# Kernel optimization log

Measured on AMD Instinct MI355X. Metric: run time of the kernel, lower is better.

## Reference

```python
import jax, jax.numpy as jnp
import numpy as np

# Dimensions
N, C, D, H = 4, 1024, 768, 12      # docs, seq_len, hidden, heads
E, M, P = 32, 4, 256               # entities/doc, mentions/entity, pairs/doc
BS, NL = 64, 97                    # block_size, num relation labels


def setup_inputs() -> dict:
    key = jax.random.key(0)
    ks = jax.random.split(key, 16)
    s = 0.02
    seq = jax.random.normal(ks[0], (N, C, D), jnp.float32)
    attn = jax.random.uniform(ks[1], (N, H, C, C), jnp.float32)
    pos = jax.random.randint(ks[2], (N, E, M), 1, C)         # mention positions (offset applied, all valid)
    hts = jax.random.randint(ks[3], (N, P, 2), 0, E)         # entity-pair indices
    return {
        'seq': seq, 'attn': attn, 'pos': pos, 'hts': hts,
        'Wq': jax.random.normal(ks[4], (D, D), jnp.float32) * s,
        'bq': jnp.zeros((D,), jnp.float32),
        'Wk': jax.random.normal(ks[5], (D, D), jnp.float32) * s,
        'bk': jnp.zeros((D,), jnp.float32),
        'aw': jax.random.normal(ks[6], (2 * D, 1), jnp.float32) * s,
        'ab': jnp.zeros((1,), jnp.float32),
        'Wh': jax.random.normal(ks[7], (3 * D, D), jnp.float32) * s,
        'bh': jnp.zeros((D,), jnp.float32),
        'Wt': jax.random.normal(ks[8], (3 * D, D), jnp.float32) * s,
        'bt': jnp.zeros((D,), jnp.float32),
        'Wb': jax.random.normal(ks[9], (D * BS, NL), jnp.float32) * s,
        'bb': jnp.zeros((NL,), jnp.float32),
    }


def mention_guide(rs, mem, mask, Wq, bq, Wk, bk, aw, ab):
    # rs: [N,P,D] query; mem: [N,P,M,D] mention embs; mask: [N,P,M] bool
    sq = rs @ Wq + bq                                  # [N,P,D]
    sk = mem @ Wk + bk                                 # [N,P,M,D]
    sq_exp = jnp.broadcast_to(sq[:, :, None, :], sk.shape)
    inp = jnp.concatenate([sq_exp, sk], axis=-1)       # [N,P,M,2D]
    scores = jax.nn.leaky_relu((inp @ aw + ab)[..., 0], 0.01)   # [N,P,M]
    scores = jnp.where(mask, scores, -1e9)
    p = jax.nn.softmax(scores, axis=-1)                # attention over mentions
    return jnp.einsum('npm,npmd->npd', p, sk)


def reference(seq, attn, pos, hts, Wq, bq, Wk, bk, aw, ab, Wh, bh, Wt, bt, Wb, bb):
    nidx = jnp.arange(N)
    # per-entity mention gather + logsumexp pooling
    ment_emb = seq[nidx[:, None, None], pos]                      # [N,E,M,D]
    ent_emb = jax.scipy.special.logsumexp(ment_emb, axis=2)       # [N,E,D]
    att_t = attn.transpose(0, 2, 1, 3)                            # [N,C,H,C]
    ent_att = att_t[nidx[:, None, None], pos].mean(axis=2)        # [N,E,H,C]

    h_idx, t_idx = hts[..., 0], hts[..., 1]
    b = nidx[:, None]
    hs = ent_emb[b, h_idx]                                        # [N,P,D]
    ts = ent_emb[b, t_idx]
    h_att = ent_att[b, h_idx]                                     # [N,P,H,C]
    t_att = ent_att[b, t_idx]
    ht_att = (h_att * t_att).mean(axis=2)                         # [N,P,C]
    ht_att = ht_att / (ht_att.sum(axis=-1, keepdims=True) + 1e-5)
    rs = jnp.einsum('ncd,npc->npd', seq, ht_att)                  # local context

    # mention-level attention for head/tail entities
    h_pos = pos[b, h_idx]                                         # [N,P,M]
    t_pos = pos[b, t_idx]
    h_embs = seq[nidx[:, None, None], h_pos]                      # [N,P,M,D]
    t_embs = seq[nidx[:, None, None], t_pos]
    hess = mention_guide(rs, h_embs, h_pos != 0, Wq, bq, Wk, bk, aw, ab)
    tess = mention_guide(rs, t_embs, t_pos != 0, Wq, bq, Wk, bk, aw, ab)

    zh = jnp.tanh(jnp.tanh(jnp.concatenate([rs, hs, hess], -1) @ Wh + bh))
    zt = jnp.tanh(jnp.concatenate([rs, ts, tess], -1) @ Wt + bt)

    # group bilinear classifier
    b1 = zh.reshape(N * P, D // BS, BS)
    b2 = zt.reshape(N * P, D // BS, BS)
    bl = (b1[:, :, :, None] * b2[:, :, None, :]).reshape(N * P, D * BS)
    return bl @ Wb + bb                                            # [N*P, NL]
```

## Files before the change

kernel.cpp:

```cpp
#include <hip/hip_runtime.h>
#include <hip/hip_bf16.h>
#include <math.h>

#define N_ 4
#define C_ 1024
#define D_ 768
#define H_ 12
#define E_ 32
#define M_ 4
#define P_ 256
#define NL_ 97
#define NLP_ 112
#define NP_ (N_*P_)
#define K3D_ 2304
#define KBL_ 49152

typedef __attribute__((ext_vector_type(8))) short short8;
typedef __attribute__((ext_vector_type(4))) float f32x4;
typedef __attribute__((ext_vector_type(4))) unsigned short ushort4v;

__device__ __forceinline__ short f2bf(float x){
  union { __hip_bfloat16 h; short s; } u; u.h = __float2bfloat16(x); return u.s;
}
__device__ __forceinline__ unsigned short f2bfu(float x){
  union { __hip_bfloat16 h; unsigned short s; } u; u.h = __float2bfloat16(x); return u.s;
}
__device__ __forceinline__ float bf2f(unsigned short u){
  union { unsigned int i; float f; } x; x.i = ((unsigned int)u)<<16; return x.f;
}

__device__ __forceinline__ float blockReduceSum256(float v){
  __shared__ float red_s[4];
  #pragma unroll
  for (int o=32;o>0;o>>=1) v += __shfl_down(v, o);
  if ((threadIdx.x & 63)==0) red_s[threadIdx.x>>6] = v;
  __syncthreads();
  float t = red_s[0]+red_s[1]+red_s[2]+red_s[3];
  __syncthreads();
  return t;
}

__device__ __forceinline__ void tcvt64(const float* __restrict__ in,
    __hip_bfloat16* __restrict__ out, int R, int C, int Cp, int tile){
  __shared__ float tb[64][33];
  const int tiles_c = (Cp + 31) >> 5;
  const int rb = (tile/tiles_c)*64, cb = (tile%tiles_c)*32;
  const int tid = threadIdx.x;
  const bool vec = ((C & 3) == 0);
  #pragma unroll
  for (int i=0;i<2;i++){
    const int idx = tid + i*256;
    const int row = idx>>3, c4 = (idx&7)*4;
    const int c = cb + c4;
    float v0=0.f,v1=0.f,v2=0.f,v3=0.f;
    if (vec && c+3 < C){
      const f32x4 v = *(const f32x4*)&in[(size_t)(rb+row)*C + c];
      v0=v[0]; v1=v[1]; v2=v[2]; v3=v[3];
    } else {
      const float* rp = in + (size_t)(rb+row)*C;
      if (c   < C) v0 = rp[c];
      if (c+1 < C) v1 = rp[c+1];
      if (c+2 < C) v2 = rp[c+2];
      if (c+3 < C) v3 = rp[c+3];
    }
    tb[row][c4]=v0; tb[row][c4+1]=v1; tb[row][c4+2]=v2; tb[row][c4+3]=v3;
  }
  __syncthreads();
  #pragma unroll
  for (int i=0;i<4;i++){
    const int idx = tid + i*256;
    const int cr = idx>>5, p = idx&31;
    const int cc = cb + cr;
    if (cc < Cp){
      union { struct { unsigned short a,b; } s; unsigned int u; } pk;
      pk.s.a = f2bfu(tb[2*p][cr]);
      pk.s.b = f2bfu(tb[2*p+1][cr]);
      *(unsigned int*)&out[(size_t)cc*R + rb + 2*p] = pk.u;
    }
  }
}

#define T_WH 864
#define T_WT 864
#define T_WK 288
#define T_WB 3072
#define T_SEQ 1536
#define O_WT  (T_WH)
#define O_WK  (O_WT+T_WT)
#define O_WB  (O_WK+T_WK)
#define O_SEQ (O_WB+T_WB)
#define O_EMB (O_SEQ+T_SEQ)
#define O_ATT (O_EMB+N_*E_)
#define O_VQ  (O_ATT+N_*E_*H_)
#define O_WKAW (O_VQ+D_)
#define O_MISC (O_WKAW+D_)
#define G_PREP (O_MISC+1)

__global__ __launch_bounds__(256) void k_prep(
    const float* __restrict__ seq, const float* __restrict__ attn,
    const int* __restrict__ pos,
    const float* __restrict__ Wq, const float* __restrict__ bq,
    const float* __restrict__ Wk, const float* __restrict__ bk,
    const float* __restrict__ aw, const float* __restrict__ ab,
    const float* __restrict__ Wh, const float* __restrict__ Wt,
    const float* __restrict__ Wb,
    __hip_bfloat16* __restrict__ WhT, __hip_bfloat16* __restrict__ WtT,
    __hip_bfloat16* __restrict__ WkT, __hip_bfloat16* __restrict__ WbT,
    __hip_bfloat16* __restrict__ seqT,
    __hip_bfloat16* __restrict__ ent_bf, __hip_bfloat16* __restrict__ Ambf,
    __hip_bfloat16* __restrict__ att_bf,
    float* __restrict__ vq, float* __restrict__ wk_aw, float* __restrict__ qc2){
  const int b = blockIdx.x;
  const int tid = threadIdx.x;
  if (b < O_WT){ tcvt64(Wh, WhT, K3D_, D_, D_, b); return; }
  if (b < O_WK){ tcvt64(Wt, WtT, K3D_, D_, D_, b-O_WT); return; }
  if (b < O_WB){ tcvt64(Wk, WkT, D_, D_, D_, b-O_WK); return; }
  if (b < O_SEQ){ tcvt64(Wb, WbT, KBL_, NL_, NLP_, b-O_WB); return; }
  if (b < O_EMB){ tcvt64(seq, seqT, N_*C_, D_, D_, b-O_SEQ); return; }
  if (b < O_ATT){
    const int be = b - O_EMB;
    const int n = be >> 5;
    const int* pp = pos + be*M_;
    if (tid < 192){
      const int c4 = tid*4;
      const f32x4 v0 = *(const f32x4*)&seq[((size_t)n*C_ + pp[0])*D_ + c4];
      const f32x4 v1 = *(const f32x4*)&seq[((size_t)n*C_ + pp[1])*D_ + c4];
      const f32x4 v2 = *(const f32x4*)&seq[((size_t)n*C_ + pp[2])*D_ + c4];
      const f32x4 v3 = *(const f32x4*)&seq[((size_t)n*C_ + pp[3])*D_ + c4];
      ushort4v a0,a1,a2,a3,e;
      #pragma unroll
      for (int j=0;j<4;j++){
        a0[j]=f2bfu(v0[j]); a1[j]=f2bfu(v1[j]); a2[j]=f2bfu(v2[j]); a3[j]=f2bfu(v3[j]);
        const float m = fmaxf(fmaxf(v0[j],v1[j]), fmaxf(v2[j],v3[j]));
        const float s = expf(v0[j]-m)+expf(v1[j]-m)+expf(v2[j]-m)+expf(v3[j]-m);
        e[j] = f2bfu(m + logf(s));
      }
      *(ushort4v*)&Ambf[(size_t)(be*4+0)*D_ + c4] = a0;
      *(ushort4v*)&Ambf[(size_t)(be*4+1)*D_ + c4] = a1;
      *(ushort4v*)&Ambf[(size_t)(be*4+2)*D_ + c4] = a2;
      *(ushort4v*)&Ambf[(size_t)(be*4+3)*D_ + c4] = a3;
      *(ushort4v*)&ent_bf[(size_t)be*D_ + c4] = e;
    }
    return;
  }
  if (b < O_VQ){
    const int bb2 = b - O_ATT;
    const int h = bb2 % H_;
    const int ne = bb2 / H_;
    const int n = ne >> 5;
    const int* pp = pos + ne*M_;
    const float* basep = attn + ((size_t)(n*H_+h))*C_*C_;
    const int c4 = tid*4;
    const f32x4 r0 = *(const f32x4*)&basep[(size_t)pp[0]*C_ + c4];
    const f32x4 r1 = *(const f32x4*)&basep[(size_t)pp[1]*C_ + c4];
    const f32x4 r2 = *(const f32x4*)&basep[(size_t)pp[2]*C_ + c4];
    const f32x4 r3 = *(const f32x4*)&basep[(size_t)pp[3]*C_ + c4];
    ushort4v o;
    #pragma unroll
    for (int j=0;j<4;j++) o[j] = f2bfu(0.25f*(r0[j]+r1[j]+r2[j]+r3[j]));
    *(ushort4v*)&att_bf[(size_t)bb2*C_ + c4] = o;
    return;
  }
  if (b < O_WKAW){
    const int k = b - O_VQ;
    float s = 0.f;
    for (int d=tid; d<D_; d+=256) s += Wq[(size_t)k*D_+d]*aw[d];
    s = blockReduceSum256(s);
    if (tid==0) vq[k] = s;
    return;
  }
  if (b < O_MISC){
    const int k = b - O_WKAW;
    float s = 0.f;
    for (int d=tid; d<D_; d+=256) s += Wk[(size_t)k*D_+d]*aw[D_+d];
    s = blockReduceSum256(s);
    if (tid==0) wk_aw[k] = s;
    return;
  }
  {
    float s0 = 0.f, s1 = 0.f;
    for (int d=tid; d<D_; d+=256){ s0 += bq[d]*aw[d]; s1 += bk[d]*aw[D_+d]; }
    s0 = blockReduceSum256(s0);
    s1 = blockReduceSum256(s1);
    if (tid==0){ qc2[0] = s0 + ab[0]; qc2[1] = s1; }
  }
}

__global__ __launch_bounds__(256) void k_ht2(
    const __hip_bfloat16* __restrict__ att_bf, const int* __restrict__ hts,
    const __hip_bfloat16* __restrict__ Ambf, const float* __restrict__ wk_aw,
    const float* __restrict__ qc2,
    __hip_bfloat16* __restrict__ ht_bf, float* __restrict__ kdot){
  const int b = blockIdx.x, tid = threadIdx.x;
  if (b < NP_){
    const int r = b, n = r >> 8;
    const int he = hts[r*2], te = hts[r*2+1];
    const unsigned short* ha = (const unsigned short*)att_bf + ((size_t)(n*E_+he))*H_*C_;
    const unsigned short* ta = (const unsigned short*)att_bf + ((size_t)(n*E_+te))*H_*C_;
    const int c0 = tid*4;
    float v[4] = {0.f,0.f,0.f,0.f};
    #pragma unroll
    for (int h=0;h<H_;h++){
      const ushort4v a = *(const ushort4v*)&ha[h*C_ + c0];
      const ushort4v t = *(const ushort4v*)&ta[h*C_ + c0];
      #pragma unroll
      for (int j=0;j<4;j++) v[j] = fmaf(bf2f(a[j]), bf2f(t[j]), v[j]);
    }
    float local = 0.f;
    #pragma unroll
    for (int j=0;j<4;j++){ v[j] *= (1.0f/H_); local += v[j]; }
    const float tot = blockReduceSum256(local);
    const float inv = 1.f/(tot + 1e-5f);
    ushort4v o;
    #pragma unroll
    for (int j=0;j<4;j++) o[j] = f2bfu(v[j]*inv);
    *(ushort4v*)&ht_bf[(size_t)r*C_ + c0] = o;
  } else {
    const int g = b - NP_;
    const unsigned short* Am = (const unsigned short*)Ambf + (size_t)g*D_;
    float s = 0.f;
    for (int d=tid; d<D_; d+=256) s += bf2f(Am[d])*wk_aw[d];
    s = blockReduceSum256(s);
    if (tid==0) kdot[g] = s + qc2[1];
  }
}

__global__ __launch_bounds__(256) void k_gemm1(
    const __hip_bfloat16* __restrict__ Ambf, const __hip_bfloat16* __restrict__ WkT,
    const float* __restrict__ bk, float* __restrict__ KK,
    const __hip_bfloat16* __restrict__ ht_bf, const __hip_bfloat16* __restrict__ seqT,
    __hip_bfloat16* __restrict__ rs_bf){
  __shared__ short As[64][136];
  __shared__ short Bs[64][136];
  const int tid = threadIdx.x;
  const int w = tid>>6, l = tid&63, wm = w>>1, wn = w&1;
  const int srow = tid>>4, sk8 = (tid&15)*8;
  const short *Ap, *Bp;
  int lda, ldb, K, bm, bn;
  bool isKK;
  if (blockIdx.x < 96){
    isKK = true;
    bm = (blockIdx.x/12)*64; bn = (blockIdx.x%12)*64;
    Ap = (const short*)Ambf + (size_t)bm*D_; lda = D_; K = D_;
    Bp = (const short*)WkT + (size_t)bn*D_;  ldb = D_;
  } else {
    isKK = false;
    const int z = blockIdx.x - 96;
    const int n = z/48, rem = z%48, bmI = rem/12, bnI = rem%12;
    bm = n*P_ + bmI*64; bn = bnI*64;
    Ap = (const short*)ht_bf + (size_t)bm*C_;            lda = C_;     K = C_;
    Bp = (const short*)seqT + (size_t)bn*(N_*C_) + n*C_; ldb = N_*C_;
  }
  short8 pA[4], pB[4];
  auto loadAB = [&](int k0){
    #pragma unroll
    for (int t=0;t<4;t++){
      const int row = srow + t*16;
      pA[t] = *(const short8*)&Ap[(size_t)row*lda + k0 + sk8];
      pB[t] = *(const short8*)&Bp[(size_t)row*ldb + k0 + sk8];
    }
  };
  loadAB(0);
  f32x4 acc[2][2] = {};
  for (int k0=0;k0<K;k0+=128){
    #pragma unroll
    for (int t=0;t<4;t++){
      *(short8*)&As[srow+t*16][sk8] = pA[t];
      *(short8*)&Bs[srow+t*16][sk8] = pB[t];
    }
    __syncthreads();
    if (k0+128 < K) loadAB(k0+128);
    #pragma unroll
    for (int h=0;h<4;h++){
      short8 af[2], bfv[2];
      #pragma unroll
      for (int f=0;f<2;f++){
        af[f]  = *(short8*)&As[wm*32+f*16+(l&15)][h*32+(l>>4)*8];
        bfv[f] = *(short8*)&Bs[wn*32+f*16+(l&15)][h*32+(l>>4)*8];
      }
      #pragma unroll
      for (int i=0;i<2;i++)
        #pragma unroll
        for (int j=0;j<2;j++)
          acc[i][j] = __builtin_amdgcn_mfma_f32_16x16x32_bf16(af[i], bfv[j], acc[i][j], 0,0,0);
    }
    __syncthreads();
  }
  #pragma unroll
  for (int i=0;i<2;i++)
    #pragma unroll
    for (int j=0;j<2;j++)
      #pragma unroll
      for (int r_=0;r_<4;r_++){
        const int row = bm + wm*32 + i*16 + (l>>4)*4 + r_;
        const int col = bn + wn*32 + j*16 + (l&15);
        const float v = acc[i][j][r_];
        if (isKK) KK[(size_t)row*D_ + col] = v + bk[col];
        else      rs_bf[(size_t)row*D_ + col] = __float2bfloat16(v);
      }
}

__global__ __launch_bounds__(256) void k_mention(
    const __hip_bfloat16* __restrict__ rs_bf, const float* __restrict__ KK,
    const float* __restrict__ vq, const float* __restrict__ qc2,
    const float* __restrict__ kdot, const int* __restrict__ pos,
    const int* __restrict__ hts,
    __hip_bfloat16* __restrict__ hess, __hip_bfloat16* __restrict__ tess){
  const int r = blockIdx.x, n = r>>8, tid = threadIdx.x;
  const unsigned short* rsp = (const unsigned short*)rs_bf + (size_t)r*D_;
  float s = 0.f;
  for (int d=tid; d<D_; d+=256) s += bf2f(rsp[d])*vq[d];
  const float q = blockReduceSum256(s) + qc2[0];
  #pragma unroll
  for (int side=0;side<2;side++){
    const int e = hts[r*2+side];
    const int base = (n*E_+e)*M_;
    float sc[4];
    #pragma unroll
    for (int m=0;m<4;m++){
      float t = q + kdot[base+m];
      t = (t > 0.f) ? t : 0.01f*t;
      sc[m] = (pos[base+m] != 0) ? t : -1e9f;
    }
    const float mx = fmaxf(fmaxf(sc[0],sc[1]), fmaxf(sc[2],sc[3]));
    float ex[4]; float sum = 0.f;
    #pragma unroll
    for (int m=0;m<4;m++){ ex[m] = expf(sc[m]-mx); sum += ex[m]; }
    const float inv = 1.f/sum;
    const float p0=ex[0]*inv, p1=ex[1]*inv, p2=ex[2]*inv, p3=ex[3]*inv;
    const float* K0 = KK + (size_t)(base+0)*D_;
    const float* K1 = KK + (size_t)(base+1)*D_;
    const float* K2 = KK + (size_t)(base+2)*D_;
    const float* K3 = KK + (size_t)(base+3)*D_;
    __hip_bfloat16* outp = (side ? tess : hess) + (size_t)r*D_;
    for (int d=tid; d<D_; d+=256)
      outp[d] = __float2bfloat16(p0*K0[d] + p1*K1[d] + p2*K2[d] + p3*K3[d]);
  }
}

__global__ __launch_bounds__(256) void k_gemm_z(
    const __hip_bfloat16* __restrict__ rs_bf, const __hip_bfloat16* __restrict__ ent_bf,
    const __hip_bfloat16* __restrict__ hess_bf, const __hip_bfloat16* __restrict__ tess_bf,
    const int* __restrict__ hts,
    const __hip_bfloat16* __restrict__ WhT, const __hip_bfloat16* __restrict__ WtT,
    const float* __restrict__ bh, const float* __restrict__ bt,
    float* __restrict__ zh, float* __restrict__ zt){
  const int side = blockIdx.z;
  const int bm = blockIdx.y*64, bn = blockIdx.x*64;
  const short* BT = (const short*)(side ? WtT : WhT);
  const float* bias = side ? bt : bh;
  float* Cm = side ? zt : zh;
  const short* hx  = (const short*)(side ? tess_bf : hess_bf);
  const short* rsp = (const short*)rs_bf;
  const short* enp = (const short*)ent_bf;
  __shared__ short As[64][136];
  __shared__ short Bs[64][136];
  __shared__ int e_s[64];
  const int tid = threadIdx.x;
  if (tid < 64) e_s[tid] = hts[(bm+tid)*2 + side];
  __syncthreads();
  const int w = tid>>6, l = tid&63, wm = w>>1, wn = w&1;
  const int srow = tid>>4, sk8 = (tid&15)*8;
  short8 pA[4], pB[4];
  auto loadAB = [&](int k0){
    #pragma unroll
    for (int t=0;t<4;t++){
      const int row = srow + t*16;
      const int arow = bm + row;
      const int gk = k0 + sk8;
      const short* src;
      if (gk < D_)        src = &rsp[(size_t)arow*D_ + gk];
      else if (gk < 2*D_) src = &enp[((size_t)(arow>>8)*E_ + e_s[row])*D_ + gk - D_];
      else                src = &hx[(size_t)arow*D_ + gk - 2*D_];
      pA[t] = *(const short8*)src;
      pB[t] = *(const short8*)&BT[(size_t)(bn+row)*K3D_ + gk];
    }
  };
  loadAB(0);
  f32x4 acc[2][2] = {};
  for (int k0=0;k0<K3D_;k0+=128){
    #pragma unroll
    for (int t=0;t<4;t++){
      *(short8*)&As[srow+t*16][sk8] = pA[t];
      *(short8*)&Bs[srow+t*16][sk8] = pB[t];
    }
    __syncthreads();
    if (k0+128 < K3D_) loadAB(k0+128);
    #pragma unroll
    for (int h=0;h<4;h++){
      short8 af[2], bfv[2];
      #pragma unroll
      for (int f=0;f<2;f++){
        af[f]  = *(short8*)&As[wm*32+f*16+(l&15)][h*32+(l>>4)*8];
        bfv[f] = *(short8*)&Bs[wn*32+f*16+(l&15)][h*32+(l>>4)*8];
      }
      #pragma unroll
      for (int i=0;i<2;i++)
        #pragma unroll
        for (int j=0;j<2;j++)
          acc[i][j] = __builtin_amdgcn_mfma_f32_16x16x32_bf16(af[i], bfv[j], acc[i][j], 0,0,0);
    }
    __syncthreads();
  }
  #pragma unroll
  for (int i=0;i<2;i++)
    #pragma unroll
    for (int j=0;j<2;j++)
      #pragma unroll
      for (int r_=0;r_<4;r_++){
        const int row = bm + wm*32 + i*16 + (l>>4)*4 + r_;
        const int col = bn + wn*32 + j*16 + (l&15);
        float v = acc[i][j][r_] + bias[col];
        v = tanhf(v);
        if (side==0) v = tanhf(v);
        Cm[(size_t)row*D_ + col] = v;
      }
}

__global__ __launch_bounds__(256) void k_bilinear(
    const float* __restrict__ zh, const float* __restrict__ zt,
    const __hip_bfloat16* __restrict__ WbT, __hip_bfloat16* __restrict__ partial){
  const int kc = blockIdx.x;
  const int blkI = kc >> 1, half = kc & 1;
  const int r0 = blockIdx.y*64;
  __shared__ float zh_s[64][36];
  __shared__ float zt_s[64][68];
  __shared__ short Bs[4][NLP_][40];
  const int tid = threadIdx.x;
  for (int idx=tid; idx<64*32; idx+=256){
    const int row = idx>>5, c = idx&31;
    zh_s[row][c] = zh[(size_t)(r0+row)*D_ + blkI*64 + half*32 + c];
  }
  for (int idx=tid; idx<64*64; idx+=256){
    const int row = idx>>6, c = idx&63;
    zt_s[row][c] = zt[(size_t)(r0+row)*D_ + blkI*64 + c];
  }
  const int w = tid>>6, l = tid&63;
  const int arow = w*16 + (l&15);
  const short* WT = (const short*)WbT;
  const size_t kbase = (size_t)blkI*4096 + half*2048;
  int sl[7], cl[7], k8l[7];
  #pragma unroll
  for (int t=0;t<7;t++){
    const int ci = tid + t*256;
    sl[t] = ci/448;
    const int rem = ci - sl[t]*448;
    cl[t] = rem>>2; k8l[t] = (rem&3)*8;
  }
  short8 pre[7];
  #pragma unroll
  for (int t=0;t<7;t++)
    pre[t] = *(const short8*)&WT[(size_t)cl[t]*KBL_ + kbase + (size_t)sl[t]*32 + k8l[t]];
  f32x4 acc[7] = {};
  for (int g=0; g<16; ++g){
    __syncthreads();
    #pragma unroll
    for (int t=0;t<7;t++) *(short8*)&Bs[sl[t]][cl[t]][k8l[t]] = pre[t];
    __syncthreads();
    if (g < 15){
      #pragma unroll
      for (int t=0;t<7;t++)
        pre[t] = *(const short8*)&WT[(size_t)cl[t]*KBL_ + kbase + (size_t)((g+1)*4+sl[t])*32 + k8l[t]];
    }
    #pragma unroll
    for (int ss=0;ss<4;ss++){
      const int s = g*4 + ss;
      const int iLoc = s>>1;
      const int jj = (s&1)*32 + (l>>4)*8;
      const float a = zh_s[arow][iLoc];
      f32x4 z0 = *(f32x4*)&zt_s[arow][jj];
      f32x4 z1 = *(f32x4*)&zt_s[arow][jj+4];
      short8 afr;
      #pragma unroll
      for (int t=0;t<4;t++) afr[t]   = f2bf(a*z0[t]);
      #pragma unroll
      for (int t=0;t<4;t++) afr[4+t] = f2bf(a*z1[t]);
      #pragma unroll
      for (int nf=0;nf<7;nf++){
        const short8 bfr = *(short8*)&Bs[ss][nf*16 + (l&15)][(l>>4)*8];
        acc[nf] = __builtin_amdgcn_mfma_f32_16x16x32_bf16(afr, bfr, acc[nf], 0,0,0);
      }
    }
  }
  unsigned short* pp = (unsigned short*)partial;
  #pragma unroll
  for (int nf=0;nf<7;nf++)
    #pragma unroll
    for (int r_=0;r_<4;r_++){
      const int row = r0 + w*16 + (l>>4)*4 + r_;
      const int col = nf*16 + (l&15);
      pp[((size_t)kc*NP_ + row)*NLP_ + col] = f2bfu(acc[nf][r_]);
    }
}

__global__ __launch_bounds__(256) void k_reduce(const __hip_bfloat16* __restrict__ partial,
    const float* __restrict__ bb, float* __restrict__ out){
  const int idx = blockIdx.x*256 + threadIdx.x;
  if (idx >= NP_*NL_) return;
  const int r = idx / NL_;
  const int l = idx - r*NL_;
  const unsigned short* pp = (const unsigned short*)partial;
  float s = bb[l];
  #pragma unroll
  for (int kc=0;kc<24;kc++) s += bf2f(pp[((size_t)kc*NP_ + r)*NLP_ + l]);
  out[idx] = s;
}

extern "C" void kernel_launch(void* const* d_in, const int* in_sizes, int n_in,
                              void* d_out, int out_size, void* d_ws, size_t ws_size,
                              hipStream_t stream){
  const float* seq  = (const float*)d_in[0];
  const float* attn = (const float*)d_in[1];
  const int*   pos  = (const int*)d_in[2];
  const int*   hts  = (const int*)d_in[3];
  const float* Wq = (const float*)d_in[4];
  const float* bq = (const float*)d_in[5];
  const float* Wk = (const float*)d_in[6];
  const float* bk = (const float*)d_in[7];
  const float* aw = (const float*)d_in[8];
  const float* ab = (const float*)d_in[9];
  const float* Wh = (const float*)d_in[10];
  const float* bh = (const float*)d_in[11];
  const float* Wt = (const float*)d_in[12];
  const float* bt = (const float*)d_in[13];
  const float* Wb = (const float*)d_in[14];
  const float* bb = (const float*)d_in[15];
  float* out = (float*)d_out;

  char* base = (char*)d_ws;
  size_t off = 0;
  auto alloc = [&](size_t bytes)->void*{
    void* p = base + off;
    off += (bytes + 255) & ~(size_t)255;
    return p;
  };
  __hip_bfloat16* WhT   = (__hip_bfloat16*)alloc((size_t)D_*K3D_*2);
  __hip_bfloat16* WtT   = (__hip_bfloat16*)alloc((size_t)D_*K3D_*2);
  __hip_bfloat16* WkT   = (__hip_bfloat16*)alloc((size_t)D_*D_*2);
  __hip_bfloat16* WbT   = (__hip_bfloat16*)alloc((size_t)NLP_*KBL_*2);
  __hip_bfloat16* seqT  = (__hip_bfloat16*)alloc((size_t)D_*N_*C_*2);
  __hip_bfloat16* ent_bf= (__hip_bfloat16*)alloc((size_t)N_*E_*D_*2);
  __hip_bfloat16* att_bf= (__hip_bfloat16*)alloc((size_t)N_*E_*H_*C_*2);
  __hip_bfloat16* ht_bf = (__hip_bfloat16*)alloc((size_t)NP_*C_*2);
  __hip_bfloat16* Ambf  = (__hip_bfloat16*)alloc((size_t)N_*E_*M_*D_*2);
  float* KK             = (float*)alloc((size_t)N_*E_*M_*D_*4);
  float* vq             = (float*)alloc(D_*4);
  float* wk_aw          = (float*)alloc(D_*4);
  float* qc2            = (float*)alloc(256);
  float* kdot           = (float*)alloc(512*4);
  __hip_bfloat16* rs_bf = (__hip_bfloat16*)alloc((size_t)NP_*D_*2);
  __hip_bfloat16* hess  = (__hip_bfloat16*)alloc((size_t)NP_*D_*2);
  __hip_bfloat16* tess  = (__hip_bfloat16*)alloc((size_t)NP_*D_*2);
  float* zh             = (float*)alloc((size_t)NP_*D_*4);
  float* zt             = (float*)alloc((size_t)NP_*D_*4);
  __hip_bfloat16* partial = (__hip_bfloat16*)alloc((size_t)24*NP_*NLP_*2);
  (void)ws_size; (void)in_sizes; (void)n_in; (void)out_size;

  k_prep<<<G_PREP, 256, 0, stream>>>(seq, attn, pos, Wq, bq, Wk, bk, aw, ab, Wh, Wt, Wb,
                                     WhT, WtT, WkT, WbT, seqT, ent_bf, Ambf, att_bf,
                                     vq, wk_aw, qc2);
  k_ht2<<<NP_ + 512, 256, 0, stream>>>(att_bf, hts, Ambf, wk_aw, qc2, ht_bf, kdot);
  k_gemm1<<<288, 256, 0, stream>>>(Ambf, WkT, bk, KK, ht_bf, seqT, rs_bf);
  k_mention<<<NP_, 256, 0, stream>>>(rs_bf, KK, vq, qc2, kdot, pos, hts, hess, tess);
  k_gemm_z<<<dim3(D_/64, NP_/64, 2), 256, 0, stream>>>(rs_bf, ent_bf, hess, tess, hts,
                                                       WhT, WtT, bh, bt, zh, zt);
  k_bilinear<<<dim3(24, NP_/64), 256, 0, stream>>>(zh, zt, WbT, partial);
  k_reduce<<<(NP_*NL_+255)/256, 256, 0, stream>>>(partial, bb, out);
}
```

Measured before the change: 105.5 us.

## Split-K the z GEMM three ways and fuse reductions into bilinear via atomics

The z projection GEMM is split along K into three partial products (rs, entity, mention segments), giving 6x more blocks. The bias, tanh and summing of the partials move into the bilinear kernel's load phase. The separate reduce kernel is removed: the bilinear kernel atomically adds fp32 results into the output, which k_mention pre-initialises with the bias. This trades an extra kernel launch and a bf16 partial buffer for more fp32 partial traffic and atomic contention, and the atomic sums make results nondeterministic.

After: 117.3 us. +11.2%, slower.

```diff
diff --git a/kernel.cpp b/kernel.cpp
--- a/kernel.cpp
+++ b/kernel.cpp
@@ -305,8 +305,10 @@
     const float* __restrict__ vq, const float* __restrict__ qc2,
     const float* __restrict__ kdot, const int* __restrict__ pos,
     const int* __restrict__ hts,
-    __hip_bfloat16* __restrict__ hess, __hip_bfloat16* __restrict__ tess){
+    __hip_bfloat16* __restrict__ hess, __hip_bfloat16* __restrict__ tess,
+    const float* __restrict__ bb, float* __restrict__ out){
   const int r = blockIdx.x, n = r>>8, tid = threadIdx.x;
+  if (tid < NL_) out[(size_t)r*NL_ + tid] = bb[tid];
   const unsigned short* rsp = (const unsigned short*)rs_bf + (size_t)r*D_;
   float s = 0.f;
   for (int d=tid; d<D_; d+=256) s += bf2f(rsp[d])*vq[d];
@@ -343,16 +345,15 @@
     const __hip_bfloat16* __restrict__ hess_bf, const __hip_bfloat16* __restrict__ tess_bf,
     const int* __restrict__ hts,
     const __hip_bfloat16* __restrict__ WhT, const __hip_bfloat16* __restrict__ WtT,
-    const float* __restrict__ bh, const float* __restrict__ bt,
-    float* __restrict__ zh, float* __restrict__ zt){
-  const int side = blockIdx.z;
+    float* __restrict__ zp){
+  const int side = blockIdx.z & 1;
+  const int ks = blockIdx.z >> 1;
   const int bm = blockIdx.y*64, bn = blockIdx.x*64;
   const short* BT = (const short*)(side ? WtT : WhT);
-  const float* bias = side ? bt : bh;
-  float* Cm = side ? zt : zh;
   const short* hx  = (const short*)(side ? tess_bf : hess_bf);
   const short* rsp = (const short*)rs_bf;
   const short* enp = (const short*)ent_bf;
+  float* Cm = zp + (size_t)(side*3 + ks)*NP_*D_;
   __shared__ short As[64][136];
   __shared__ short Bs[64][136];
   __shared__ int e_s[64];
@@ -369,23 +370,23 @@
       const int arow = bm + row;
       const int gk = k0 + sk8;
       const short* src;
-      if (gk < D_)        src = &rsp[(size_t)arow*D_ + gk];
-      else if (gk < 2*D_) src = &enp[((size_t)(arow>>8)*E_ + e_s[row])*D_ + gk - D_];
-      else                src = &hx[(size_t)arow*D_ + gk - 2*D_];
+      if (ks == 0)      src = &rsp[(size_t)arow*D_ + gk];
+      else if (ks == 1) src = &enp[((size_t)(arow>>8)*E_ + e_s[row])*D_ + gk];
+      else              src = &hx[(size_t)arow*D_ + gk];
       pA[t] = *(const short8*)src;
-      pB[t] = *(const short8*)&BT[(size_t)(bn+row)*K3D_ + gk];
+      pB[t] = *(const short8*)&BT[(size_t)(bn+row)*K3D_ + ks*D_ + gk];
     }
   };
   loadAB(0);
   f32x4 acc[2][2] = {};
-  for (int k0=0;k0<K3D_;k0+=128){
+  for (int k0=0;k0<D_;k0+=128){
     #pragma unroll
     for (int t=0;t<4;t++){
       *(short8*)&As[srow+t*16][sk8] = pA[t];
       *(short8*)&Bs[srow+t*16][sk8] = pB[t];
     }
     __syncthreads();
-    if (k0+128 < K3D_) loadAB(k0+128);
+    if (k0+128 < D_) loadAB(k0+128);
     #pragma unroll
     for (int h=0;h<4;h++){
       short8 af[2], bfv[2];
@@ -410,16 +411,14 @@
       for (int r_=0;r_<4;r_++){
         const int row = bm + wm*32 + i*16 + (l>>4)*4 + r_;
         const int col = bn + wn*32 + j*16 + (l&15);
-        float v = acc[i][j][r_] + bias[col];
-        v = tanhf(v);
-        if (side==0) v = tanhf(v);
-        Cm[(size_t)row*D_ + col] = v;
+        Cm[(size_t)row*D_ + col] = acc[i][j][r_];
       }
 }
 
 __global__ __launch_bounds__(256) void k_bilinear(
-    const float* __restrict__ zh, const float* __restrict__ zt,
-    const __hip_bfloat16* __restrict__ WbT, __hip_bfloat16* __restrict__ partial){
+    const float* __restrict__ zp,
+    const float* __restrict__ bh, const float* __restrict__ bt,
+    const __hip_bfloat16* __restrict__ WbT, float* __restrict__ out){
   const int kc = blockIdx.x;
   const int blkI = kc >> 1, half = kc & 1;
   const int r0 = blockIdx.y*64;
@@ -427,13 +426,23 @@
   __shared__ float zt_s[64][68];
   __shared__ short Bs[4][NLP_][40];
   const int tid = threadIdx.x;
+  const size_t S = (size_t)NP_*D_;
+  const float* zph = zp;
+  const float* zpt = zp + 3*S;
   for (int idx=tid; idx<64*32; idx+=256){
     const int row = idx>>5, c = idx&31;
-    zh_s[row][c] = zh[(size_t)(r0+row)*D_ + blkI*64 + half*32 + c];
+    const int col = blkI*64 + half*32 + c;
+    const size_t o = (size_t)(r0+row)*D_ + col;
+    float s = zph[o] + zph[S+o] + zph[2*S+o] + bh[col];
+    s = tanhf(tanhf(s));
+    zh_s[row][c] = s;
   }
   for (int idx=tid; idx<64*64; idx+=256){
     const int row = idx>>6, c = idx&63;
-    zt_s[row][c] = zt[(size_t)(r0+row)*D_ + blkI*64 + c];
+    const int col = blkI*64 + c;
+    const size_t o = (size_t)(r0+row)*D_ + col;
+    float s = zpt[o] + zpt[S+o] + zpt[2*S+o] + bt[col];
+    zt_s[row][c] = tanhf(s);
   }
   const int w = tid>>6, l = tid&63;
   const int arow = w*16 + (l&15);
@@ -482,28 +491,15 @@
       }
     }
   }
-  unsigned short* pp = (unsigned short*)partial;
   #pragma unroll
   for (int nf=0;nf<7;nf++)
     #pragma unroll
     for (int r_=0;r_<4;r_++){
       const int row = r0 + w*16 + (l>>4)*4 + r_;
       const int col = nf*16 + (l&15);
-      pp[((size_t)kc*NP_ + row)*NLP_ + col] = f2bfu(acc[nf][r_]);
-    }
-}
-
-__global__ __launch_bounds__(256) void k_reduce(const __hip_bfloat16* __restrict__ partial,
-    const float* __restrict__ bb, float* __restrict__ out){
-  const int idx = blockIdx.x*256 + threadIdx.x;
-  if (idx >= NP_*NL_) return;
-  const int r = idx / NL_;
-  const int l = idx - r*NL_;
-  const unsigned short* pp = (const unsigned short*)partial;
-  float s = bb[l];
-  #pragma unroll
-  for (int kc=0;kc<24;kc++) s += bf2f(pp[((size_t)kc*NP_ + r)*NLP_ + l]);
-  out[idx] = s;
+      if (col < NL_)
+        atomicAdd(&out[(size_t)row*NL_ + col], acc[nf][r_]);
+    }
 }
 
 extern "C" void kernel_launch(void* const* d_in, const int* in_sizes, int n_in,
@@ -551,9 +547,7 @@
   __hip_bfloat16* rs_bf = (__hip_bfloat16*)alloc((size_t)NP_*D_*2);
   __hip_bfloat16* hess  = (__hip_bfloat16*)alloc((size_t)NP_*D_*2);
   __hip_bfloat16* tess  = (__hip_bfloat16*)alloc((size_t)NP_*D_*2);
-  float* zh             = (float*)alloc((size_t)NP_*D_*4);
-  float* zt             = (float*)alloc((size_t)NP_*D_*4);
-  __hip_bfloat16* partial = (__hip_bfloat16*)alloc((size_t)24*NP_*NLP_*2);
+  float* zp             = (float*)alloc((size_t)6*NP_*D_*4);
   (void)ws_size; (void)in_sizes; (void)n_in; (void)out_size;
 
   k_prep<<<G_PREP, 256, 0, stream>>>(seq, attn, pos, Wq, bq, Wk, bk, aw, ab, Wh, Wt, Wb,
@@ -561,9 +555,8 @@
                                      vq, wk_aw, qc2);
   k_ht2<<<NP_ + 512, 256, 0, stream>>>(att_bf, hts, Ambf, wk_aw, qc2, ht_bf, kdot);
   k_gemm1<<<288, 256, 0, stream>>>(Ambf, WkT, bk, KK, ht_bf, seqT, rs_bf);
-  k_mention<<<NP_, 256, 0, stream>>>(rs_bf, KK, vq, qc2, kdot, pos, hts, hess, tess);
-  k_gemm_z<<<dim3(D_/64, NP_/64, 2), 256, 0, stream>>>(rs_bf, ent_bf, hess, tess, hts,
-                                                       WhT, WtT, bh, bt, zh, zt);
-  k_bilinear<<<dim3(24, NP_/64), 256, 0, stream>>>(zh, zt, WbT, partial);
-  k_reduce<<<(NP_*NL_+255)/256, 256, 0, stream>>>(partial, bb, out);
-}
+  k_mention<<<NP_, 256, 0, stream>>>(rs_bf, KK, vq, qc2, kdot, pos, hts, hess, tess, bb, out);
+  k_gemm_z<<<dim3(D_/64, NP_/64, 6), 256, 0, stream>>>(rs_bf, ent_bf, hess, tess, hts,
+                                                       WhT, WtT, zp);
+  k_bilinear<<<dim3(24, NP_/64), 256, 0, stream>>>(zp, bh, bt, WbT, out);
+}
```
